# Kernel optimization log

Hardware: AMD Instinct MI355X
Metric: run time of the kernel (lower is better)

The kernel has to match this reference:

```python
import jax, jax.numpy as jnp
import numpy as np

NUM_TABLES = 26
VOCAB = 100000
D = 128          # sparse_feature_size == mlp_bot[-1]
B = 8192
P = 10           # fixed pooling factor per bag
DENSE = 13
BOT = [512, 256, 128]
TOP = [1024, 1024, 512, 256, 1]
NF = NUM_TABLES + 1  # features entering dot interaction


def setup_inputs() -> dict:
    key = jax.random.key(0)
    ks = iter(jax.random.split(key, 32))
    inp = {}
    inp["dense_x"] = jax.random.normal(next(ks), (B, DENSE), dtype=jnp.float32)
    inp["sparse_indices"] = jax.random.randint(next(ks), (NUM_TABLES, B * P), 0, VOCAB, dtype=jnp.int32)
    # EmbeddingBag weights init: uniform(-0.01, 0.01)
    inp["emb_tables"] = jax.random.uniform(next(ks), (NUM_TABLES, VOCAB, D), jnp.float32, -0.01, 0.01)
    def xavier(k, shape):
        fan_out, fan_in = shape
        lim = np.sqrt(6.0 / (fan_in + fan_out)).astype(np.float32)
        return jax.random.uniform(k, shape, jnp.float32, -lim, lim)
    dims_bot = [DENSE] + BOT
    for i in range(len(BOT)):
        inp[f"bot_w{i}"] = xavier(next(ks), (dims_bot[i + 1], dims_bot[i]))
        inp[f"bot_b{i}"] = jnp.zeros((dims_bot[i + 1],), jnp.float32)
    interact_dim = NF * (NF - 1) // 2 + BOT[-1]  # 351 + 128 = 479
    dims_top = [interact_dim] + TOP
    for i in range(len(TOP)):
        inp[f"top_w{i}"] = xavier(next(ks), (dims_top[i + 1], dims_top[i]))
        inp[f"top_b{i}"] = jnp.zeros((dims_top[i + 1],), jnp.float32)
    return inp


def reference(dense_x, sparse_indices, emb_tables,
              bot_w0, bot_b0, bot_w1, bot_b1, bot_w2, bot_b2,
              top_w0, top_b0, top_w1, top_b1, top_w2, top_b2,
              top_w3, top_b3, top_w4, top_b4):
    # bottom MLP (Linear + ReLU on every layer)
    x = dense_x
    for w, b in ((bot_w0, bot_b0), (bot_w1, bot_b1), (bot_w2, bot_b2)):
        x = jax.nn.relu(x @ w.T + b)  # [B, 128]

    # multi-table EmbeddingBag sum pooling (fixed pooling factor P)
    idx = sparse_indices.reshape(NUM_TABLES, B, P)
    ly = jax.vmap(lambda tab, i: tab[i].sum(axis=1))(emb_tables, idx)  # [T, B, D]

    # dot interaction: bmm + upper-triangular gather
    T_feat = jnp.concatenate([x[None], ly], axis=0).transpose(1, 0, 2)  # [B, NF, D]
    Z = jnp.einsum('bnd,bmd->bnm', T_feat, T_feat)                       # [B, NF, NF]
    li, lj = np.triu_indices(NF, k=1)
    Zflat = Z[:, li, lj]                                                 # [B, NF*(NF-1)/2]
    z = jnp.concatenate([x, Zflat], axis=1)                              # [B, 479]

    # top MLP: ReLU on all but last layer
    h = z
    tops = ((top_w0, top_b0), (top_w1, top_b1), (top_w2, top_b2), (top_w3, top_b3))
    for w, b in tops:
        h = jax.nn.relu(h @ w.T + b)
    p = h @ top_w4.T + top_b4  # [B, 1]
    return jax.nn.sigmoid(p.squeeze(1))
```

## Files before the change

kernel.cpp:

```cpp
#include <hip/hip_runtime.h>
#include <hip/hip_bf16.h>
#include <cstdint>

typedef __attribute__((ext_vector_type(8))) short bf16x8;
typedef __attribute__((ext_vector_type(4))) float f32x4;

#define B_SZ 8192
#define NF 27
#define TROW 3456

__device__ __forceinline__ void gld_lds16(const void* g, void* l) {
    __builtin_amdgcn_global_load_lds(
        (const __attribute__((address_space(1))) unsigned int*)g,
        (__attribute__((address_space(3))) unsigned int*)l, 16, 0, 0);
}

struct CvtJob { const float* in; __hip_bfloat16* out; int N, K, Kp; };
struct CvtJobs { CvtJob j[8]; int start[9]; };

__global__ __launch_bounds__(256) void cvt_all(CvtJobs jobs) {
    int gid = blockIdx.x * 256 + threadIdx.x;
    if (gid >= jobs.start[8]) return;
    int k = 0;
    #pragma unroll
    for (int i = 1; i < 8; i++) if (gid >= jobs.start[i]) k = i;
    const CvtJob& J = jobs.j[k];
    int local = gid - jobs.start[k];
    int n = local / J.Kp, kk = local - n * J.Kp;
    float v = (kk < J.K) ? J.in[(size_t)n * J.K + kk] : 0.f;
    J.out[local] = __float2bfloat16(v);
}

__global__ __launch_bounds__(256) void emb_kernel(const int* __restrict__ idx,
                                                  const float* __restrict__ tab,
                                                  __hip_bfloat16* __restrict__ T) {
    int lane = threadIdx.x & 63, wv = threadIdx.x >> 6;
    int p = blockIdx.x * 4 + wv;
    int t = p >> 13;
    int b = p & 8191;
    const int* ip = idx + (size_t)t * 81920 + b * 10;
    const float* tb = tab + (size_t)t * 100000 * 128;
    float ax = 0.f, ay = 0.f;
    #pragma unroll
    for (int j = 0; j < 10; j++) {
        int r = ip[j];
        const float2* src = (const float2*)(tb + (size_t)r * 128) + lane;
        float2 v = *src;
        ax += v.x; ay += v.y;
    }
    __hip_bfloat162 o;
    o.x = __float2bfloat16(ax);
    o.y = __float2bfloat16(ay);
    ((__hip_bfloat162*)(T + (size_t)b * TROW + (1 + t) * 128))[lane] = o;
}

template<int TM, int TN, int WM, int WN, int RELU>
__global__ __launch_bounds__(256) void gemm_t(const __hip_bfloat16* __restrict__ A,
                                              const __hip_bfloat16* __restrict__ W,
                                              const float* __restrict__ bias,
                                              __hip_bfloat16* __restrict__ C,
                                              int M, int N, int K, int ldc) {
    constexpr int ROWS = TM + TN;
    constexpr int CH = ROWS * 4 / 256;
    constexpr int MI = TM / WM / 16;
    constexpr int NI = TN / WN / 16;
    __shared__ __align__(16) __hip_bfloat16 ABs[ROWS * 32];

    const int tid = threadIdx.x;
    const int lane = tid & 63, wave = tid >> 6;
    const int wmI = wave / WN, wnI = wave % WN;
    const int m0 = blockIdx.y * TM, n0 = blockIdx.x * TN;

    const __hip_bfloat16* gp[CH];
    #pragma unroll
    for (int c = 0; c < CH; c++) {
        int gid = c * 256 + tid;
        int row = gid >> 2, col = (gid & 3) * 8;
        gp[c] = (row < TM ? A + (size_t)(m0 + row) * K
                          : W + (size_t)(n0 + row - TM) * K) + col;
    }

    f32x4 acc[MI][NI] = {};
    const int fr = lane & 15, fkb = (lane >> 4) * 8;

    for (int k0 = 0; k0 < K; k0 += 32) {
        __syncthreads();
        #pragma unroll
        for (int c = 0; c < CH; c++)
            gld_lds16(gp[c] + k0, &ABs[(c * 256 + wave * 64) * 8]);
        asm volatile("s_waitcnt vmcnt(0)" ::: "memory");
        __syncthreads();
        bf16x8 a[MI], b[NI];
        #pragma unroll
        for (int i = 0; i < MI; i++)
            a[i] = *(const bf16x8*)&ABs[(wmI * (TM / WM) + i * 16 + fr) * 32 + fkb];
        #pragma unroll
        for (int j = 0; j < NI; j++)
            b[j] = *(const bf16x8*)&ABs[(TM + wnI * (TN / WN) + j * 16 + fr) * 32 + fkb];
        #pragma unroll
        for (int i = 0; i < MI; i++)
            #pragma unroll
            for (int j = 0; j < NI; j++)
                acc[i][j] = __builtin_amdgcn_mfma_f32_16x16x32_bf16(a[i], b[j], acc[i][j], 0, 0, 0);
    }

    const int fq = lane >> 4;
    #pragma unroll
    for (int i = 0; i < MI; i++) {
        #pragma unroll
        for (int j = 0; j < NI; j++) {
            int n = n0 + wnI * (TN / WN) + j * 16 + fr;
            float bv = bias[n];
            #pragma unroll
            for (int r = 0; r < 4; r++) {
                int m = m0 + wmI * (TM / WM) + i * 16 + fq * 4 + r;
                float v = acc[i][j][r] + bv;
                if (RELU) v = fmaxf(v, 0.f);
                C[(size_t)m * ldc + n] = __float2bfloat16(v);
            }
        }
    }
}

__global__ __launch_bounds__(256) void interact_kernel(const __hip_bfloat16* __restrict__ T,
                                                       __hip_bfloat16* __restrict__ z) {
    __shared__ __align__(16) __hip_bfloat16 S[4][32 * 128];
    int lane = threadIdx.x & 63, wave = threadIdx.x >> 6;
    int b = blockIdx.x * 4 + wave;
    __hip_bfloat16* Sw = S[wave];
    const uint4* src = (const uint4*)(T + (size_t)b * TROW);
    uint4* dst = (uint4*)Sw;
    for (int i = lane; i < 432; i += 64) dst[i] = src[i];
    uint4 z4 = {0u, 0u, 0u, 0u};
    for (int i = 432 + lane; i < 512; i += 64) dst[i] = z4;
    __syncthreads();

    const int fr = lane & 15, fkb = (lane >> 4) * 8;
    bf16x8 fr2[2][4];
    #pragma unroll
    for (int mi = 0; mi < 2; mi++)
        #pragma unroll
        for (int kt = 0; kt < 4; kt++)
            fr2[mi][kt] = *(const bf16x8*)&Sw[(mi * 16 + fr) * 128 + kt * 32 + fkb];

    f32x4 acc[2][2] = {};
    #pragma unroll
    for (int kt = 0; kt < 4; kt++)
        #pragma unroll
        for (int mi = 0; mi < 2; mi++)
            #pragma unroll
            for (int ni = 0; ni < 2; ni++)
                acc[mi][ni] = __builtin_amdgcn_mfma_f32_16x16x32_bf16(fr2[mi][kt], fr2[ni][kt], acc[mi][ni], 0, 0, 0);

    __hip_bfloat16* zb = z + (size_t)b * 512;
    zb[lane] = Sw[lane];
    zb[64 + lane] = Sw[64 + lane];
    if (lane < 33) zb[479 + lane] = __float2bfloat16(0.f);
    const int fq = lane >> 4;
    #pragma unroll
    for (int mi = 0; mi < 2; mi++) {
        #pragma unroll
        for (int ni = 0; ni < 2; ni++) {
            #pragma unroll
            for (int r = 0; r < 4; r++) {
                int m = mi * 16 + fq * 4 + r;
                int n = ni * 16 + fr;
                if (m < 27 && n < 27 && m < n) {
                    int p = m * 26 - (m * (m - 1)) / 2 + (n - m - 1);
                    zb[128 + p] = __float2bfloat16(acc[mi][ni][r]);
                }
            }
        }
    }
}

__global__ __launch_bounds__(256) void final_kernel(const __hip_bfloat16* __restrict__ h,
                                                    const float* __restrict__ w,
                                                    const float* __restrict__ bias,
                                                    float* __restrict__ out) {
    int lane = threadIdx.x & 63, wv = threadIdx.x >> 6;
    int s = blockIdx.x * 4 + wv;
    const __hip_bfloat16* hp = h + (size_t)s * 256;
    float sum = 0.f;
    #pragma unroll
    for (int i = 0; i < 4; i++) {
        int k = i * 64 + lane;
        sum += __bfloat162float(hp[k]) * w[k];
    }
    #pragma unroll
    for (int off = 32; off; off >>= 1) sum += __shfl_down(sum, off, 64);
    if (lane == 0) out[s] = 1.f / (1.f + expf(-(sum + bias[0])));
}

extern "C" void kernel_launch(void* const* d_in, const int* in_sizes, int n_in,
                              void* d_out, int out_size, void* d_ws, size_t ws_size,
                              hipStream_t stream) {
    const float* dense_x = (const float*)d_in[0];
    const int* sidx      = (const int*)d_in[1];
    const float* emb     = (const float*)d_in[2];
    const float* bw0 = (const float*)d_in[3];  const float* bb0 = (const float*)d_in[4];
    const float* bw1 = (const float*)d_in[5];  const float* bb1 = (const float*)d_in[6];
    const float* bw2 = (const float*)d_in[7];  const float* bb2 = (const float*)d_in[8];
    const float* tw0 = (const float*)d_in[9];  const float* tb0 = (const float*)d_in[10];
    const float* tw1 = (const float*)d_in[11]; const float* tb1 = (const float*)d_in[12];
    const float* tw2 = (const float*)d_in[13]; const float* tb2 = (const float*)d_in[14];
    const float* tw3 = (const float*)d_in[15]; const float* tb3 = (const float*)d_in[16];
    const float* tw4 = (const float*)d_in[17]; const float* tb4 = (const float*)d_in[18];
    float* out = (float*)d_out;

    char* ws = (char*)d_ws;
    size_t off = 0;
    auto alloc = [&](size_t bytes) {
        off = (off + 255) & ~(size_t)255;
        void* p = ws + off;
        off += bytes;
        return p;
    };
    __hip_bfloat16* A0  = (__hip_bfloat16*)alloc((size_t)B_SZ * 32 * 2);
    __hip_bfloat16* Wb0 = (__hip_bfloat16*)alloc((size_t)512 * 32 * 2);
    __hip_bfloat16* Wb1 = (__hip_bfloat16*)alloc((size_t)256 * 512 * 2);
    __hip_bfloat16* Wb2 = (__hip_bfloat16*)alloc((size_t)128 * 256 * 2);
    __hip_bfloat16* Wt0 = (__hip_bfloat16*)alloc((size_t)1024 * 512 * 2);
    __hip_bfloat16* Wt1 = (__hip_bfloat16*)alloc((size_t)1024 * 1024 * 2);
    __hip_bfloat16* Wt2 = (__hip_bfloat16*)alloc((size_t)512 * 1024 * 2);
    __hip_bfloat16* Wt3 = (__hip_bfloat16*)alloc((size_t)256 * 512 * 2);
    __hip_bfloat16* bufA = (__hip_bfloat16*)alloc((size_t)B_SZ * 1024 * 2);
    __hip_bfloat16* bufB = (__hip_bfloat16*)alloc((size_t)B_SZ * 1024 * 2);
    __hip_bfloat16* Tbuf = (__hip_bfloat16*)alloc((size_t)B_SZ * TROW * 2);
    __hip_bfloat16* zbuf = (__hip_bfloat16*)alloc((size_t)B_SZ * 512 * 2);

    CvtJobs cj;
    auto setJob = [&](int i, const float* in, __hip_bfloat16* o, int N, int K, int Kp) {
        cj.j[i] = {in, o, N, K, Kp};
    };
    setJob(0, dense_x, A0, B_SZ, 13, 32);
    setJob(1, bw0, Wb0, 512, 13, 32);
    setJob(2, bw1, Wb1, 256, 512, 512);
    setJob(3, bw2, Wb2, 128, 256, 256);
    setJob(4, tw0, Wt0, 1024, 479, 512);
    setJob(5, tw1, Wt1, 1024, 1024, 1024);
    setJob(6, tw2, Wt2, 512, 1024, 1024);
    setJob(7, tw3, Wt3, 256, 512, 512);
    cj.start[0] = 0;
    for (int i = 0; i < 8; i++) cj.start[i + 1] = cj.start[i] + cj.j[i].N * cj.j[i].Kp;
    int totalCvt = cj.start[8];
    cvt_all<<<(totalCvt + 255) / 256, 256, 0, stream>>>(cj);

    gemm_t<128,128,2,2,1><<<dim3(512/128, B_SZ/128), 256, 0, stream>>>(A0, Wb0, bb0, bufA, B_SZ, 512, 32, 512);
    gemm_t<128, 64,2,2,1><<<dim3(256/ 64, B_SZ/128), 256, 0, stream>>>(bufA, Wb1, bb1, bufB, B_SZ, 256, 512, 256);
    gemm_t< 64, 64,2,2,1><<<dim3(128/ 64, B_SZ/ 64), 256, 0, stream>>>(bufB, Wb2, bb2, Tbuf, B_SZ, 128, 256, TROW);

    emb_kernel<<<26 * B_SZ / 4, 256, 0, stream>>>(sidx, emb, Tbuf);

    interact_kernel<<<B_SZ / 4, 256, 0, stream>>>(Tbuf, zbuf);

    gemm_t<128,128,2,2,1><<<dim3(1024/128, B_SZ/128), 256, 0, stream>>>(zbuf, Wt0, tb0, bufA, B_SZ, 1024, 512, 1024);
    gemm_t<128,128,2,2,1><<<dim3(1024/128, B_SZ/128), 256, 0, stream>>>(bufA, Wt1, tb1, bufB, B_SZ, 1024, 1024, 1024);
    gemm_t<128, 64,2,2,1><<<dim3( 512/ 64, B_SZ/128), 256, 0, stream>>>(bufB, Wt2, tb2, bufA, B_SZ, 512, 1024, 512);
    gemm_t<128, 64,2,2,1><<<dim3( 256/ 64, B_SZ/128), 256, 0, stream>>>(bufA, Wt3, tb3, bufB, B_SZ, 256, 512, 256);

    final_kernel<<<B_SZ / 4, 256, 0, stream>>>(bufB, tw4, tb4, out);
}
```

Baseline: 337.4 us.

## Fuse first bottom layer into conversion kernel, drop LDS staging in interaction

Merges weight conversion (now 8-wide vectorised) with a scalar FP32 computation of the first bottom MLP layer in one launch, removing the dense input conversion and its GEMM. The interaction kernel loads MFMA fragments directly from global memory instead of staging through shared memory. Top MLP GEMMs switch to 128x64 tiles with separate output buffers. Padding rows in the interaction now read neighbouring data rather than zeros, which affects only discarded outputs.

```diff
diff --git a/kernel.cpp b/kernel.cpp
--- a/kernel.cpp
+++ b/kernel.cpp
@@ -6,7 +6,6 @@
 typedef __attribute__((ext_vector_type(4))) float f32x4;
 
 #define B_SZ 8192
-#define NF 27
 #define TROW 3456
 
 __device__ __forceinline__ void gld_lds16(const void* g, void* l) {
@@ -15,20 +14,65 @@
         (__attribute__((address_space(3))) unsigned int*)l, 16, 0, 0);
 }
 
+__device__ __forceinline__ short f2bf_bits(float v) {
+    return __builtin_bit_cast(short, __float2bfloat16(v));
+}
+
 struct CvtJob { const float* in; __hip_bfloat16* out; int N, K, Kp; };
-struct CvtJobs { CvtJob j[8]; int start[9]; };
-
-__global__ __launch_bounds__(256) void cvt_all(CvtJobs jobs) {
-    int gid = blockIdx.x * 256 + threadIdx.x;
-    if (gid >= jobs.start[8]) return;
+struct CvtJobs { CvtJob j[6]; int start[7]; };
+
+__device__ __forceinline__ void cvt_dev8(int lb, int tid, const CvtJobs& J) {
+    int chunk = lb * 256 + tid;
+    int e = chunk * 8;
+    if (e >= J.start[6]) return;
     int k = 0;
     #pragma unroll
-    for (int i = 1; i < 8; i++) if (gid >= jobs.start[i]) k = i;
-    const CvtJob& J = jobs.j[k];
-    int local = gid - jobs.start[k];
-    int n = local / J.Kp, kk = local - n * J.Kp;
-    float v = (kk < J.K) ? J.in[(size_t)n * J.K + kk] : 0.f;
-    J.out[local] = __float2bfloat16(v);
+    for (int i = 1; i < 6; i++) if (e >= J.start[i]) k = i;
+    const CvtJob& job = J.j[k];
+    int local = e - J.start[k];
+    float v[8];
+    if (job.K == job.Kp) {
+        const float4* p = (const float4*)(job.in + local);
+        float4 a = p[0], b = p[1];
+        v[0]=a.x; v[1]=a.y; v[2]=a.z; v[3]=a.w; v[4]=b.x; v[5]=b.y; v[6]=b.z; v[7]=b.w;
+    } else {
+        int n = local / job.Kp, kk = local - n * job.Kp;
+        #pragma unroll
+        for (int i = 0; i < 8; i++)
+            v[i] = (kk + i < job.K) ? job.in[(size_t)n * job.K + kk + i] : 0.f;
+    }
+    bf16x8 o;
+    #pragma unroll
+    for (int i = 0; i < 8; i++)
+        o[i] = f2bf_bits(v[i]);
+    *(bf16x8*)(job.out + local) = o;
+}
+
+__device__ __forceinline__ void bot0_dev(int lb, int tid, const float* __restrict__ x,
+    const float* __restrict__ w, const float* __restrict__ bias,
+    __hip_bfloat16* __restrict__ o, float* xs) {
+    int m0 = lb * 4;
+    if (tid < 52) xs[tid] = x[(size_t)m0 * 13 + tid];
+    __syncthreads();
+    for (int c = tid; c < 512; c += 256) {
+        const float* wr = w + (size_t)c * 13;
+        float bv = bias[c];
+        #pragma unroll
+        for (int r = 0; r < 4; r++) {
+            float s = bv;
+            #pragma unroll
+            for (int k = 0; k < 13; k++) s += xs[r * 13 + k] * wr[k];
+            o[(size_t)(m0 + r) * 512 + c] = __float2bfloat16(fmaxf(s, 0.f));
+        }
+    }
+}
+
+__global__ __launch_bounds__(256) void k_pre(CvtJobs J, int cvtB,
+    const float* dx, const float* w0, const float* b0, __hip_bfloat16* bufA) {
+    __shared__ float xs[64];
+    int blk = blockIdx.x, tid = threadIdx.x;
+    if (blk < cvtB) { cvt_dev8(blk, tid, J); return; }
+    bot0_dev(blk - cvtB, tid, dx, w0, b0, bufA, xs);
 }
 
 __global__ __launch_bounds__(256) void emb_kernel(const int* __restrict__ idx,
@@ -44,8 +88,7 @@
     #pragma unroll
     for (int j = 0; j < 10; j++) {
         int r = ip[j];
-        const float2* src = (const float2*)(tb + (size_t)r * 128) + lane;
-        float2 v = *src;
+        float2 v = ((const float2*)(tb + (size_t)r * 128))[lane];
         ax += v.x; ay += v.y;
     }
     __hip_bfloat162 o;
@@ -54,7 +97,7 @@
     ((__hip_bfloat162*)(T + (size_t)b * TROW + (1 + t) * 128))[lane] = o;
 }
 
-template<int TM, int TN, int WM, int WN, int RELU>
+template<int TM, int TN, int WM, int WN>
 __global__ __launch_bounds__(256) void gemm_t(const __hip_bfloat16* __restrict__ A,
                                               const __hip_bfloat16* __restrict__ W,
                                               const float* __restrict__ bias,
@@ -114,26 +157,17 @@
             #pragma unroll
             for (int r = 0; r < 4; r++) {
                 int m = m0 + wmI * (TM / WM) + i * 16 + fq * 4 + r;
-                float v = acc[i][j][r] + bv;
-                if (RELU) v = fmaxf(v, 0.f);
-                C[(size_t)m * ldc + n] = __float2bfloat16(v);
+                C[(size_t)m * ldc + n] = __float2bfloat16(fmaxf(acc[i][j][r] + bv, 0.f));
             }
         }
     }
 }
 
-__global__ __launch_bounds__(256) void interact_kernel(const __hip_bfloat16* __restrict__ T,
-                                                       __hip_bfloat16* __restrict__ z) {
-    __shared__ __align__(16) __hip_bfloat16 S[4][32 * 128];
+__global__ __launch_bounds__(256) void k_int(const __hip_bfloat16* __restrict__ T,
+                                             __hip_bfloat16* __restrict__ z) {
     int lane = threadIdx.x & 63, wave = threadIdx.x >> 6;
     int b = blockIdx.x * 4 + wave;
-    __hip_bfloat16* Sw = S[wave];
-    const uint4* src = (const uint4*)(T + (size_t)b * TROW);
-    uint4* dst = (uint4*)Sw;
-    for (int i = lane; i < 432; i += 64) dst[i] = src[i];
-    uint4 z4 = {0u, 0u, 0u, 0u};
-    for (int i = 432 + lane; i < 512; i += 64) dst[i] = z4;
-    __syncthreads();
+    const __hip_bfloat16* Tb = T + (size_t)b * TROW;
 
     const int fr = lane & 15, fkb = (lane >> 4) * 8;
     bf16x8 fr2[2][4];
@@ -141,7 +175,7 @@
     for (int mi = 0; mi < 2; mi++)
         #pragma unroll
         for (int kt = 0; kt < 4; kt++)
-            fr2[mi][kt] = *(const bf16x8*)&Sw[(mi * 16 + fr) * 128 + kt * 32 + fkb];
+            fr2[mi][kt] = *(const bf16x8*)&Tb[(mi * 16 + fr) * 128 + kt * 32 + fkb];
 
     f32x4 acc[2][2] = {};
     #pragma unroll
@@ -153,14 +187,13 @@
                 acc[mi][ni] = __builtin_amdgcn_mfma_f32_16x16x32_bf16(fr2[mi][kt], fr2[ni][kt], acc[mi][ni], 0, 0, 0);
 
     __hip_bfloat16* zb = z + (size_t)b * 512;
-    zb[lane] = Sw[lane];
-    zb[64 + lane] = Sw[64 + lane];
+    ((unsigned*)zb)[lane] = ((const unsigned*)Tb)[lane];
     if (lane < 33) zb[479 + lane] = __float2bfloat16(0.f);
     const int fq = lane >> 4;
     #pragma unroll
-    for (int mi = 0; mi < 2; mi++) {
-        #pragma unroll
-        for (int ni = 0; ni < 2; ni++) {
+    for (int mi = 0; mi < 2; mi++)
+        #pragma unroll
+        for (int ni = 0; ni < 2; ni++)
             #pragma unroll
             for (int r = 0; r < 4; r++) {
                 int m = mi * 16 + fq * 4 + r;
@@ -170,8 +203,6 @@
                     zb[128 + p] = __float2bfloat16(acc[mi][ni][r]);
                 }
             }
-        }
-    }
 }
 
 __global__ __launch_bounds__(256) void final_kernel(const __hip_bfloat16* __restrict__ h,
@@ -216,48 +247,48 @@
         off += bytes;
         return p;
     };
-    __hip_bfloat16* A0  = (__hip_bfloat16*)alloc((size_t)B_SZ * 32 * 2);
-    __hip_bfloat16* Wb0 = (__hip_bfloat16*)alloc((size_t)512 * 32 * 2);
     __hip_bfloat16* Wb1 = (__hip_bfloat16*)alloc((size_t)256 * 512 * 2);
     __hip_bfloat16* Wb2 = (__hip_bfloat16*)alloc((size_t)128 * 256 * 2);
     __hip_bfloat16* Wt0 = (__hip_bfloat16*)alloc((size_t)1024 * 512 * 2);
     __hip_bfloat16* Wt1 = (__hip_bfloat16*)alloc((size_t)1024 * 1024 * 2);
     __hip_bfloat16* Wt2 = (__hip_bfloat16*)alloc((size_t)512 * 1024 * 2);
     __hip_bfloat16* Wt3 = (__hip_bfloat16*)alloc((size_t)256 * 512 * 2);
-    __hip_bfloat16* bufA = (__hip_bfloat16*)alloc((size_t)B_SZ * 1024 * 2);
-    __hip_bfloat16* bufB = (__hip_bfloat16*)alloc((size_t)B_SZ * 1024 * 2);
+    __hip_bfloat16* bufA = (__hip_bfloat16*)alloc((size_t)B_SZ * 512 * 2);
+    __hip_bfloat16* bufB = (__hip_bfloat16*)alloc((size_t)B_SZ * 256 * 2);
     __hip_bfloat16* Tbuf = (__hip_bfloat16*)alloc((size_t)B_SZ * TROW * 2);
     __hip_bfloat16* zbuf = (__hip_bfloat16*)alloc((size_t)B_SZ * 512 * 2);
-
-    CvtJobs cj;
+    __hip_bfloat16* h0   = (__hip_bfloat16*)alloc((size_t)B_SZ * 1024 * 2);
+    __hip_bfloat16* h1   = (__hip_bfloat16*)alloc((size_t)B_SZ * 1024 * 2);
+    __hip_bfloat16* h2   = (__hip_bfloat16*)alloc((size_t)B_SZ * 512 * 2);
+    __hip_bfloat16* h3   = (__hip_bfloat16*)alloc((size_t)B_SZ * 256 * 2);
+
+    CvtJobs J;
     auto setJob = [&](int i, const float* in, __hip_bfloat16* o, int N, int K, int Kp) {
-        cj.j[i] = {in, o, N, K, Kp};
+        J.j[i] = {in, o, N, K, Kp};
     };
-    setJob(0, dense_x, A0, B_SZ, 13, 32);
-    setJob(1, bw0, Wb0, 512, 13, 32);
-    setJob(2, bw1, Wb1, 256, 512, 512);
-    setJob(3, bw2, Wb2, 128, 256, 256);
-    setJob(4, tw0, Wt0, 1024, 479, 512);
-    setJob(5, tw1, Wt1, 1024, 1024, 1024);
-    setJob(6, tw2, Wt2, 512, 1024, 1024);
-    setJob(7, tw3, Wt3, 256, 512, 512);
-    cj.start[0] = 0;
-    for (int i = 0; i < 8; i++) cj.start[i + 1] = cj.start[i] + cj.j[i].N * cj.j[i].Kp;
-    int totalCvt = cj.start[8];
-    cvt_all<<<(totalCvt + 255) / 256, 256, 0, stream>>>(cj);
-
-    gemm_t<128,128,2,2,1><<<dim3(512/128, B_SZ/128), 256, 0, stream>>>(A0, Wb0, bb0, bufA, B_SZ, 512, 32, 512);
-    gemm_t<128, 64,2,2,1><<<dim3(256/ 64, B_SZ/128), 256, 0, stream>>>(bufA, Wb1, bb1, bufB, B_SZ, 256, 512, 256);
-    gemm_t< 64, 64,2,2,1><<<dim3(128/ 64, B_SZ/ 64), 256, 0, stream>>>(bufB, Wb2, bb2, Tbuf, B_SZ, 128, 256, TROW);
+    setJob(0, bw1, Wb1, 256, 512, 512);
+    setJob(1, bw2, Wb2, 128, 256, 256);
+    setJob(2, tw0, Wt0, 1024, 479, 512);
+    setJob(3, tw1, Wt1, 1024, 1024, 1024);
+    setJob(4, tw2, Wt2, 512, 1024, 1024);
+    setJob(5, tw3, Wt3, 256, 512, 512);
+    J.start[0] = 0;
+    for (int i = 0; i < 6; i++) J.start[i + 1] = J.start[i] + J.j[i].N * J.j[i].Kp;
+    const int cvtB = (J.start[6] / 8 + 255) / 256;
+
+    k_pre<<<cvtB + B_SZ / 4, 256, 0, stream>>>(J, cvtB, dense_x, bw0, bb0, bufA);
 
     emb_kernel<<<26 * B_SZ / 4, 256, 0, stream>>>(sidx, emb, Tbuf);
 
-    interact_kernel<<<B_SZ / 4, 256, 0, stream>>>(Tbuf, zbuf);
-
-    gemm_t<128,128,2,2,1><<<dim3(1024/128, B_SZ/128), 256, 0, stream>>>(zbuf, Wt0, tb0, bufA, B_SZ, 1024, 512, 1024);
-    gemm_t<128,128,2,2,1><<<dim3(1024/128, B_SZ/128), 256, 0, stream>>>(bufA, Wt1, tb1, bufB, B_SZ, 1024, 1024, 1024);
-    gemm_t<128, 64,2,2,1><<<dim3( 512/ 64, B_SZ/128), 256, 0, stream>>>(bufB, Wt2, tb2, bufA, B_SZ, 512, 1024, 512);
-    gemm_t<128, 64,2,2,1><<<dim3( 256/ 64, B_SZ/128), 256, 0, stream>>>(bufA, Wt3, tb3, bufB, B_SZ, 256, 512, 256);
-
-    final_kernel<<<B_SZ / 4, 256, 0, stream>>>(bufB, tw4, tb4, out);
-}
+    gemm_t<128, 64, 2, 2><<<dim3(256 / 64, B_SZ / 128), 256, 0, stream>>>(bufA, Wb1, bb1, bufB, B_SZ, 256, 512, 256);
+    gemm_t< 64, 64, 2, 2><<<dim3(128 / 64, B_SZ /  64), 256, 0, stream>>>(bufB, Wb2, bb2, Tbuf, B_SZ, 128, 256, TROW);
+
+    k_int<<<B_SZ / 4, 256, 0, stream>>>(Tbuf, zbuf);
+
+    gemm_t<128, 64, 2, 2><<<dim3(1024 / 64, B_SZ / 128), 256, 0, stream>>>(zbuf, Wt0, tb0, h0, B_SZ, 1024, 512, 1024);
+    gemm_t<128, 64, 2, 2><<<dim3(1024 / 64, B_SZ / 128), 256, 0, stream>>>(h0, Wt1, tb1, h1, B_SZ, 1024, 1024, 1024);
+    gemm_t<128, 64, 2, 2><<<dim3( 512 / 64, B_SZ / 128), 256, 0, stream>>>(h1, Wt2, tb2, h2, B_SZ, 512, 1024, 512);
+    gemm_t<128, 64, 2, 2><<<dim3( 256 / 64, B_SZ / 128), 256, 0, stream>>>(h2, Wt3, tb3, h3, B_SZ, 256, 512, 256);
+
+    final_kernel<<<B_SZ / 4, 256, 0, stream>>>(h3, tw4, tb4, out);
+}
```

Measured after the change: 326.5 us. 1.03x faster.
